# Optimization experiments

Measured on AMD Instinct MI355X. Metric: run time of the kernel, lower is better.

## Reference

```python
import jax, jax.numpy as jnp
import numpy as np

COLOR_CODE_NUMBER = 9

def _conv(x, w, b):
    # NCHW conv, 3x3, stride 1, padding 1 (SAME)
    y = jax.lax.conv_general_dilated(x, w, (1, 1), 'SAME',
                                     dimension_numbers=('NCHW', 'OIHW', 'NCHW'))
    return y + b[None, :, None, None]

def setup_inputs() -> dict:
    key = jax.random.key(0)
    ks = jax.random.split(key, 10)
    C, H, W = 256, 256, 256
    ms = 32
    s = 0.02
    x = jax.random.normal(ks[0], (1, C, H, W), dtype=jnp.float32)
    masks = jax.random.randint(ks[1], (COLOR_CODE_NUMBER, H, W), 0, 2, dtype=jnp.int32)
    w1 = jax.random.normal(ks[2], (128, 256, 3, 3), dtype=jnp.float32) * s
    b1 = jnp.zeros((128,), jnp.float32)
    w2 = jax.random.normal(ks[3], (64, 128, 3, 3), dtype=jnp.float32) * s
    b2 = jnp.zeros((64,), jnp.float32)
    w3 = jax.random.normal(ks[4], (ms, 64, 3, 3), dtype=jnp.float32) * s
    b3 = jnp.zeros((ms,), jnp.float32)
    fc_w = jax.random.normal(ks[5], (ms * ms, ms * ms), dtype=jnp.float32) * s
    fc_b = jnp.zeros((ms * ms,), jnp.float32)
    return {'x': x, 'masks': masks, 'w1': w1, 'b1': b1, 'w2': w2, 'b2': b2,
            'w3': w3, 'b3': b3, 'fc_w': fc_w, 'fc_b': fc_b}

def reference(x, masks, w1, b1, w2, b2, w3, b3, fc_w, fc_b):
    xb, xc, xh, xw = x.shape
    N = xh * xw
    K = masks.shape[0]
    xv = x.reshape(xc, N)                       # [C, N]
    m = masks.reshape(K, N)                     # [K, N] int
    fg = (m > 0).astype(x.dtype)                # [K, N]
    counts = fg.sum(axis=1)                     # [K]
    valid = counts >= 10.0                      # sum(mask) >= 10 for binary masks
    # per-mask gather -> mean-subtract -> scatter (sequential: later masks overwrite)
    fsm = xv
    for i in range(min(COLOR_CODE_NUMBER, K)):
        mean = (xv * fg[i]).sum(axis=1) / jnp.maximum(counts[i], 1.0)   # [C]
        sub = jnp.where(fg[i][None, :] > 0, xv - mean[:, None], fsm)
        fsm = jnp.where(valid[i], sub, fsm)
    # conv stack on mean-subtracted feature
    feat = fsm.reshape(xb, xc, xh, xw)
    feat = jax.nn.relu(_conv(feat, w1, b1))
    feat = jax.nn.relu(_conv(feat, w2, b2))
    feat = _conv(feat, w3, b3)                  # [1, ms, H, W]
    c = feat.shape[1]
    fv = feat.reshape(c, N)                     # [ms, N]
    # per-mask covariance + fc (vectorized over the 9 masks)
    fg1 = (m == 1).astype(feat.dtype)           # [K, N]
    cnt1 = fg1.sum(axis=1)                      # [K]
    masked = fv[None, :, :] * fg1[:, None, :]   # [K, ms, N]
    cov = jnp.einsum('kcn,kdn->kcd', masked, masked) / jnp.maximum(cnt1, 1.0)[:, None, None]
    trans = cov.reshape(K, c * c) @ fc_w.T + fc_b[None, :]              # [K, ms*ms]
    trans = jnp.where((cnt1 >= 10.0)[:, None], trans, jnp.zeros_like(trans))
    return trans, fsm
```

## Files before the change

kernel.cpp:

```cpp
#include <hip/hip_runtime.h>
#include <stdint.h>

#define N_PIX 65536
#define KM 9

typedef __bf16  bf16x8 __attribute__((ext_vector_type(8)));
typedef float   f32x4  __attribute__((ext_vector_type(4)));
typedef unsigned short ushort;

__device__ __forceinline__ ushort f2bf(float f) {
    uint32_t u = __builtin_bit_cast(uint32_t, f);
    uint32_t r = (u + 0x7FFFu + ((u >> 16) & 1u)) >> 16;
    return (ushort)r;
}

#define WS_BITS  0u
#define WS_CNT   262144u
#define WS_CNT1  262208u
#define WS_SUMS  262272u
#define WS_MEANS 271488u
#define WS_W1T   282624u
#define WS_W2T   872448u
#define WS_W3T   1019904u
#define WS_COV   1056768u
#define WS_XPAD  2097152u
#define WS_FV    2097152u
#define WS_PART  12582912u
#define WS_C1PAD 36173824u
#define WS_C2PAD 53212160u

template<int C>
__global__ void k_ring(ushort* p) {
    constexpr int CU = C / 2;
    int i = blockIdx.x * 256 + threadIdx.x;
    if (i >= 1028 * CU) return;
    int c = i % CU, px = i / CU;
    int row, col;
    if      (px < 258) { row = 0;   col = px; }
    else if (px < 516) { row = 257; col = px - 258; }
    else if (px < 772) { row = px - 516 + 1; col = 0; }
    else               { row = px - 772 + 1; col = 257; }
    ((uint32_t*)p)[(row * 258 + col) * CU + c] = 0u;
}

__global__ void k_pack(const int* __restrict__ masks, uint32_t* __restrict__ bits,
                       int* __restrict__ counts, int* __restrict__ cnt1) {
    int n = blockIdx.x * 256 + threadIdx.x;
    uint32_t fg = 0, f1 = 0;
#pragma unroll
    for (int k = 0; k < KM; ++k) {
        int m = masks[k * N_PIX + n];
        fg |= (uint32_t)(m > 0) << k;
        f1 |= (uint32_t)(m == 1) << k;
    }
    bits[n] = fg | (f1 << 16);
#pragma unroll
    for (int k = 0; k < KM; ++k) {
        unsigned long long b0 = __ballot((fg >> k) & 1);
        unsigned long long b1 = __ballot((f1 >> k) & 1);
        if ((threadIdx.x & 63) == 0) {
            atomicAdd(&counts[k], __popcll(b0));
            atomicAdd(&cnt1[k], __popcll(b1));
        }
    }
}

__global__ void k_sums(const float* __restrict__ x, const uint32_t* __restrict__ bits,
                       float* __restrict__ sums) {
    int c = blockIdx.x >> 4;
    int base = (blockIdx.x & 15) * 4096;
    float acc[KM];
#pragma unroll
    for (int k = 0; k < KM; ++k) acc[k] = 0.0f;
    const float* xc = x + (size_t)c * N_PIX;
    for (int i = 0; i < 16; ++i) {
        int px = base + i * 256 + threadIdx.x;
        float xv = xc[px];
        uint32_t b = bits[px];
#pragma unroll
        for (int k = 0; k < KM; ++k) acc[k] += ((b >> k) & 1) ? xv : 0.0f;
    }
#pragma unroll
    for (int k = 0; k < KM; ++k) {
        float v = acc[k];
        for (int off = 32; off; off >>= 1) v += __shfl_down(v, off);
        if ((threadIdx.x & 63) == 0) atomicAdd(&sums[k * 256 + c], v);
    }
}

__global__ void k_means(const float* __restrict__ sums, const int* __restrict__ counts,
                        float* __restrict__ means) {
    int k = blockIdx.x, c = threadIdx.x;
    means[k * 256 + c] = sums[k * 256 + c] / fmaxf((float)counts[k], 1.0f);
}

__global__ void k_fsm(const float* __restrict__ x, const uint32_t* __restrict__ bits,
                      const int* __restrict__ counts, const float* __restrict__ means,
                      float* __restrict__ fsm, ushort* __restrict__ xpad) {
    __shared__ float mst[256 * 12];
    int tid = threadIdx.x;
    for (int t = tid; t < KM * 256; t += 256) {
        int k = t >> 8, c = t & 255;
        mst[c * 12 + k] = means[t];
    }
    __syncthreads();
    uint32_t vm = 0;
#pragma unroll
    for (int k = 0; k < KM; ++k) vm |= (uint32_t)(counts[k] >= 10) << k;
    int px = blockIdx.x * 256 + tid;
    int c0 = blockIdx.y * 128;
    uint32_t sel = bits[px] & vm & 0x1FFu;
    int kl = 0; float have = 0.0f;
    if (sel) { kl = 31 - __clz((int)sel); have = 1.0f; }
    int y = px >> 8, xx = px & 255;
    size_t pbase = ((size_t)(y + 1) * 258 + (xx + 1)) * 256;
    for (int cb = 0; cb < 128; cb += 8) {
        int c = c0 + cb;
        uint32_t pk[4];
#pragma unroll
        for (int j = 0; j < 8; j += 2) {
            float v0 = x[(size_t)(c + j) * N_PIX + px]     - have * mst[(c + j) * 12 + kl];
            float v1 = x[(size_t)(c + j + 1) * N_PIX + px] - have * mst[(c + j + 1) * 12 + kl];
            fsm[(size_t)(c + j) * N_PIX + px] = v0;
            fsm[(size_t)(c + j + 1) * N_PIX + px] = v1;
            pk[j >> 1] = (uint32_t)f2bf(v0) | ((uint32_t)f2bf(v1) << 16);
        }
        uint4 w; w.x = pk[0]; w.y = pk[1]; w.z = pk[2]; w.w = pk[3];
        *(uint4*)&xpad[pbase + c] = w;
    }
}

__global__ void k_wpack(const float* __restrict__ w, ushort* __restrict__ wt,
                        int total, int OC, int IC) {
    int idx = blockIdx.x * 256 + threadIdx.x;
    if (idx >= total) return;
    int oc = idx / IC, ic = idx - oc * IC;
    const float* src = w + (size_t)idx * 9;
#pragma unroll
    for (int t = 0; t < 9; ++t)
        wt[((size_t)t * OC + oc) * IC + ic] = f2bf(src[t]);
}

template<int IC, int OC, int NT, int PXG, bool RELU, bool F32OUT>
__global__ __launch_bounds__(256) void k_convm(const ushort* __restrict__ xin,
                                               const ushort* __restrict__ wt,
                                               const float* __restrict__ bias,
                                               ushort* __restrict__ ypad,
                                               float* __restrict__ yf) {
    constexpr int NC   = IC / 32;
    constexpr int BPX  = 32 * PXG;
    constexpr int SEG  = 256 / BPX;
    constexpr int PXP  = BPX + 2;
    constexpr int RW   = PXP * 4;
    constexpr int UNITS = 3 * RW;
    constexpr int NCH  = (UNITS + 63) / 64;
    constexpr int NV   = (NCH + 3) / 4;
    static_assert(OC == 16 * NT * (4 / PXG), "tile mismatch");

    __shared__ ushort xs[NCH * 512];

    const int tid = threadIdx.x, lane = tid & 63, wv = tid >> 6;
    const int lo = lane & 15, kg = lane >> 4;
    const int y0 = blockIdx.x / SEG;
    const int x0 = (blockIdx.x % SEG) * BPX;
    const int wvpx = (wv % PXG) * 32;
    const int oc0  = (wv / PXG) * 16 * NT;

    uint32_t voff[NV];
#pragma unroll
    for (int j = 0; j < NV; ++j) {
        int ch = wv + j * 4;
        int u = ch * 64 + lane;
        u = (u < UNITS) ? u : (UNITS - 1);
        int row = u / RW;
        int rem = u - row * RW;
        int px = rem >> 2, icg = rem & 3;
        voff[j] = (uint32_t)(((y0 + row) * 258 + (x0 + px)) * IC + icg * 8);
    }

    const ushort* wlane = wt + (size_t)(oc0 + lo) * IC + kg * 8;
    const int abase = (wvpx + lo) * 32 + kg * 8;

    f32x4 acc[2][NT];
#pragma unroll
    for (int m = 0; m < 2; ++m)
#pragma unroll
        for (int n = 0; n < NT; ++n) acc[m][n] = (f32x4){0.f, 0.f, 0.f, 0.f};
    float bs[NT];
#pragma unroll
    for (int n = 0; n < NT; ++n) bs[n] = bias[oc0 + n * 16 + lo];

    uint4 sreg[NV];
#pragma unroll
    for (int j = 0; j < NV; ++j)
        if (wv + j * 4 < NCH) sreg[j] = *(const uint4*)(xin + voff[j]);

    for (int icc = 0; icc < NC; ++icc) {
#pragma unroll
        for (int j = 0; j < NV; ++j) {
            int ch = wv + j * 4;
            if (ch < NCH) *(uint4*)(xs + ch * 512 + lane * 8) = sreg[j];
        }
        __syncthreads();
        bf16x8 wf[9][NT];
#pragma unroll
        for (int tap = 0; tap < 9; ++tap)
#pragma unroll
            for (int n = 0; n < NT; ++n)
                wf[tap][n] = __builtin_bit_cast(bf16x8,
                    *(const uint4*)(wlane + ((size_t)tap * OC + n * 16) * IC + icc * 32));
        if (icc + 1 < NC) {
#pragma unroll
            for (int j = 0; j < NV; ++j)
                if (wv + j * 4 < NCH)
                    sreg[j] = *(const uint4*)(xin + voff[j] + (icc + 1) * 32);
        }
#pragma unroll
        for (int tr = 0; tr < 3; ++tr)
#pragma unroll
            for (int tc = 0; tc < 3; ++tc) {
                bf16x8 a0 = __builtin_bit_cast(bf16x8,
                    *(const uint4*)(xs + abase + (tr * PXP + tc) * 32));
                bf16x8 a1 = __builtin_bit_cast(bf16x8,
                    *(const uint4*)(xs + abase + (tr * PXP + tc) * 32 + 512));
#pragma unroll
                for (int n = 0; n < NT; ++n) {
                    acc[0][n] = __builtin_amdgcn_mfma_f32_16x16x32_bf16(a0, wf[tr * 3 + tc][n], acc[0][n], 0, 0, 0);
                    acc[1][n] = __builtin_amdgcn_mfma_f32_16x16x32_bf16(a1, wf[tr * 3 + tc][n], acc[1][n], 0, 0, 0);
                }
            }
        __syncthreads();
    }
#pragma unroll
    for (int m = 0; m < 2; ++m) {
        int pxl = x0 + wvpx + m * 16 + kg * 4;
#pragma unroll
        for (int n = 0; n < NT; ++n) {
            int oc = oc0 + n * 16 + lo;
#pragma unroll
            for (int r = 0; r < 4; ++r) {
                float v = acc[m][n][r] + bs[n];
                if (RELU) v = fmaxf(v, 0.0f);
                if (F32OUT) yf[((size_t)y0 * 256 + pxl + r) * OC + oc] = v;
                else        ypad[((size_t)(y0 + 1) * 258 + (pxl + r) + 1) * OC + oc] = f2bf(v);
            }
        }
    }
}

__global__ __launch_bounds__(256) void k_cov(const float* __restrict__ fv,
                                             const uint32_t* __restrict__ bits,
                                             float* __restrict__ part) {
    __shared__ float sf[32 * 257];
    __shared__ uint32_t sb[256];
    int px0 = blockIdx.x * 256;
    int tid = threadIdx.x;
    const float4* src = (const float4*)(fv + (size_t)(px0 + tid) * 32);
#pragma unroll
    for (int q = 0; q < 8; ++q) {
        float4 v = src[q];
        sf[(q * 4 + 0) * 257 + tid] = v.x;
        sf[(q * 4 + 1) * 257 + tid] = v.y;
        sf[(q * 4 + 2) * 257 + tid] = v.z;
        sf[(q * 4 + 3) * 257 + tid] = v.w;
    }
    sb[tid] = bits[px0 + tid] >> 16;
    __syncthreads();
    int c = tid >> 3;
    int d4 = (tid & 7) * 4;
    float a[KM][4];
#pragma unroll
    for (int k = 0; k < KM; ++k)
#pragma unroll
        for (int j = 0; j < 4; ++j) a[k][j] = 0.0f;
#pragma unroll 2
    for (int px = 0; px < 256; ++px) {
        float fc = sf[c * 257 + px];
        float f0 = sf[(d4 + 0) * 257 + px];
        float f1 = sf[(d4 + 1) * 257 + px];
        float f2 = sf[(d4 + 2) * 257 + px];
        float f3 = sf[(d4 + 3) * 257 + px];
        uint32_t b = sb[px];
#pragma unroll
        for (int k = 0; k < KM; ++k) {
            float fm = ((b >> k) & 1) ? fc : 0.0f;
            a[k][0] = fmaf(fm, f0, a[k][0]);
            a[k][1] = fmaf(fm, f1, a[k][1]);
            a[k][2] = fmaf(fm, f2, a[k][2]);
            a[k][3] = fmaf(fm, f3, a[k][3]);
        }
    }
    float* po = part + (size_t)blockIdx.x * 9216 + (c * 32 + d4);
#pragma unroll
    for (int k = 0; k < KM; ++k)
#pragma unroll
        for (int j = 0; j < 4; ++j) po[k * 1024 + j] = a[k][j];
}

__global__ void k_covred(const float* __restrict__ part, float* __restrict__ cov) {
    int p = blockIdx.x * 256 + threadIdx.x;
    float s = 0.0f;
    for (int b = 0; b < 256; ++b) s += part[(size_t)b * 9216 + p];
    cov[p] = s;
}

__global__ void k_fc(const float* __restrict__ cov, const int* __restrict__ cnt1,
                     const float* __restrict__ fcw, const float* __restrict__ fcb,
                     float* __restrict__ trans) {
    int k = blockIdx.x;
    int j = blockIdx.y * 256 + threadIdx.x;
    __shared__ float sc[1024];
    int c1 = cnt1[k];
    float inv = 1.0f / fmaxf((float)c1, 1.0f);
    for (int t = threadIdx.x; t < 1024; t += 256) sc[t] = cov[k * 1024 + t] * inv;
    __syncthreads();
    const float4* wrow = (const float4*)(fcw + (size_t)j * 1024);
    float acc = fcb[j];
#pragma unroll 4
    for (int i4 = 0; i4 < 256; ++i4) {
        float4 wv = wrow[i4];
        acc += sc[i4 * 4 + 0] * wv.x + sc[i4 * 4 + 1] * wv.y +
               sc[i4 * 4 + 2] * wv.z + sc[i4 * 4 + 3] * wv.w;
    }
    trans[k * 1024 + j] = (c1 >= 10) ? acc : 0.0f;
}

extern "C" void kernel_launch(void* const* d_in, const int* in_sizes, int n_in,
                              void* d_out, int out_size, void* d_ws, size_t ws_size,
                              hipStream_t stream) {
    const float* x     = (const float*)d_in[0];
    const int*   masks = (const int*)  d_in[1];
    const float* w1    = (const float*)d_in[2];
    const float* b1    = (const float*)d_in[3];
    const float* w2    = (const float*)d_in[4];
    const float* b2    = (const float*)d_in[5];
    const float* w3    = (const float*)d_in[6];
    const float* b3    = (const float*)d_in[7];
    const float* fcw   = (const float*)d_in[8];
    const float* fcb   = (const float*)d_in[9];

    float* out   = (float*)d_out;
    float* trans = out;
    float* fsm   = out + KM * 1024;

    char* ws = (char*)d_ws;
    uint32_t* bits = (uint32_t*)(ws + WS_BITS);
    int*   counts  = (int*)  (ws + WS_CNT);
    int*   cnt1    = (int*)  (ws + WS_CNT1);
    float* sums    = (float*)(ws + WS_SUMS);
    float* means   = (float*)(ws + WS_MEANS);
    ushort* w1t = (ushort*)(ws + WS_W1T);
    ushort* w2t = (ushort*)(ws + WS_W2T);
    ushort* w3t = (ushort*)(ws + WS_W3T);
    float* cov     = (float*)(ws + WS_COV);
    ushort* xpad  = (ushort*)(ws + WS_XPAD);
    ushort* c1pad = (ushort*)(ws + WS_C1PAD);
    ushort* c2pad = (ushort*)(ws + WS_C2PAD);
    float* fv      = (float*)(ws + WS_FV);
    float* part    = (float*)(ws + WS_PART);

    hipMemsetAsync(ws + WS_CNT, 0, 64 + 64 + 9216, stream);

    k_ring<256><<<(1028 * 128 + 255) / 256, 256, 0, stream>>>(xpad);
    k_ring<128><<<(1028 *  64 + 255) / 256, 256, 0, stream>>>(c1pad);
    k_ring< 64><<<(1028 *  32 + 255) / 256, 256, 0, stream>>>(c2pad);

    k_wpack<<<128, 256, 0, stream>>>(w1, w1t, 128 * 256, 128, 256);
    k_wpack<<< 32, 256, 0, stream>>>(w2, w2t,  64 * 128,  64, 128);
    k_wpack<<<  8, 256, 0, stream>>>(w3, w3t,  32 *  64,  32,  64);

    k_pack <<<256, 256, 0, stream>>>(masks, bits, counts, cnt1);
    k_sums <<<4096, 256, 0, stream>>>(x, bits, sums);
    k_means<<<KM, 256, 0, stream>>>(sums, counts, means);
    k_fsm  <<<dim3(256, 2), 256, 0, stream>>>(x, bits, counts, means, fsm, xpad);

    k_convm<256, 128, 4, 2, true,  false><<<1024, 256, 0, stream>>>(xpad,  w1t, b1, c1pad, nullptr);
    k_convm<128,  64, 4, 4, true,  false><<< 512, 256, 0, stream>>>(c1pad, w2t, b2, c2pad, nullptr);
    k_convm< 64,  32, 2, 4, false, true ><<< 512, 256, 0, stream>>>(c2pad, w3t, b3, nullptr, fv);

    k_cov   <<<256, 256, 0, stream>>>(fv, bits, part);
    k_covred<<<36, 256, 0, stream>>>(part, cov);
    k_fc    <<<dim3(KM, 4), 256, 0, stream>>>(cov, cnt1, fcw, fcb, trans);
}
```

Baseline: 705.6 us.

## Stream conv weight fragments with double buffer and retile conv2/conv3 to 64px blocks

The conv kernel stops preloading all nine taps of weight fragments into registers. It keeps a two-slot rolling buffer, loading the fragment for tap+2 while tap computes, and adds a launch bound of 4 blocks per CU to raise occupancy. Every layer now uses a fixed 64-pixel by 2-oc-group tiling, so conv2 and conv3 launch 1024 blocks with smaller NT. Fewer registers per thread in exchange for weight loads that sit closer to their use, which may expose latency, and more input halo reloads for the smaller layers.

New measurement: 680.9 us. -3.5%, faster.

```diff
diff --git a/kernel.cpp b/kernel.cpp
--- a/kernel.cpp
+++ b/kernel.cpp
@@ -141,30 +141,28 @@
         wt[((size_t)t * OC + oc) * IC + ic] = f2bf(src[t]);
 }
 
-template<int IC, int OC, int NT, int PXG, bool RELU, bool F32OUT>
-__global__ __launch_bounds__(256) void k_convm(const ushort* __restrict__ xin,
-                                               const ushort* __restrict__ wt,
-                                               const float* __restrict__ bias,
-                                               ushort* __restrict__ ypad,
-                                               float* __restrict__ yf) {
-    constexpr int NC   = IC / 32;
-    constexpr int BPX  = 32 * PXG;
-    constexpr int SEG  = 256 / BPX;
-    constexpr int PXP  = BPX + 2;
-    constexpr int RW   = PXP * 4;
+template<int IC, int OC, int NT, bool RELU, bool F32OUT>
+__global__ __launch_bounds__(256, 4) void k_convm(const ushort* __restrict__ xin,
+                                                  const ushort* __restrict__ wt,
+                                                  const float* __restrict__ bias,
+                                                  ushort* __restrict__ ypad,
+                                                  float* __restrict__ yf) {
+    constexpr int NC  = IC / 32;
+    constexpr int PXP = 66;
+    constexpr int RW  = PXP * 4;
     constexpr int UNITS = 3 * RW;
-    constexpr int NCH  = (UNITS + 63) / 64;
-    constexpr int NV   = (NCH + 3) / 4;
-    static_assert(OC == 16 * NT * (4 / PXG), "tile mismatch");
+    constexpr int NCH = (UNITS + 63) / 64;
+    constexpr int NV  = (NCH + 3) / 4;
+    static_assert(OC == NT * 32, "2 oc-groups of 16*NT");
 
     __shared__ ushort xs[NCH * 512];
 
     const int tid = threadIdx.x, lane = tid & 63, wv = tid >> 6;
     const int lo = lane & 15, kg = lane >> 4;
-    const int y0 = blockIdx.x / SEG;
-    const int x0 = (blockIdx.x % SEG) * BPX;
-    const int wvpx = (wv % PXG) * 32;
-    const int oc0  = (wv / PXG) * 16 * NT;
+    const int y0 = blockIdx.x >> 2;
+    const int x0 = (blockIdx.x & 3) << 6;
+    const int wvpx = (wv & 1) << 5;
+    const int oc0  = (wv >> 1) * NT * 16;
 
     uint32_t voff[NV];
 #pragma unroll
@@ -202,33 +200,40 @@
             if (ch < NCH) *(uint4*)(xs + ch * 512 + lane * 8) = sreg[j];
         }
         __syncthreads();
-        bf16x8 wf[9][NT];
-#pragma unroll
-        for (int tap = 0; tap < 9; ++tap)
-#pragma unroll
-            for (int n = 0; n < NT; ++n)
-                wf[tap][n] = __builtin_bit_cast(bf16x8,
-                    *(const uint4*)(wlane + ((size_t)tap * OC + n * 16) * IC + icc * 32));
         if (icc + 1 < NC) {
 #pragma unroll
             for (int j = 0; j < NV; ++j)
                 if (wv + j * 4 < NCH)
                     sreg[j] = *(const uint4*)(xin + voff[j] + (icc + 1) * 32);
         }
-#pragma unroll
-        for (int tr = 0; tr < 3; ++tr)
-#pragma unroll
-            for (int tc = 0; tc < 3; ++tc) {
-                bf16x8 a0 = __builtin_bit_cast(bf16x8,
-                    *(const uint4*)(xs + abase + (tr * PXP + tc) * 32));
-                bf16x8 a1 = __builtin_bit_cast(bf16x8,
-                    *(const uint4*)(xs + abase + (tr * PXP + tc) * 32 + 512));
+        const ushort* wicc = wlane + icc * 32;
+        uint4 wb0[NT], wb1[NT];
+#pragma unroll
+        for (int n = 0; n < NT; ++n) {
+            wb0[n] = *(const uint4*)(wicc + ((size_t)0 * OC + n * 16) * IC);
+            wb1[n] = *(const uint4*)(wicc + ((size_t)1 * OC + n * 16) * IC);
+        }
+#pragma unroll
+        for (int tap = 0; tap < 9; ++tap) {
+            const int tr = tap / 3, tc = tap % 3;
+            bf16x8 a0 = __builtin_bit_cast(bf16x8,
+                *(const uint4*)(xs + abase + (tr * PXP + tc) * 32));
+            bf16x8 a1 = __builtin_bit_cast(bf16x8,
+                *(const uint4*)(xs + abase + (tr * PXP + tc) * 32 + 512));
+#pragma unroll
+            for (int n = 0; n < NT; ++n) {
+                bf16x8 wfr = __builtin_bit_cast(bf16x8, (tap & 1) ? wb1[n] : wb0[n]);
+                acc[0][n] = __builtin_amdgcn_mfma_f32_16x16x32_bf16(a0, wfr, acc[0][n], 0, 0, 0);
+                acc[1][n] = __builtin_amdgcn_mfma_f32_16x16x32_bf16(a1, wfr, acc[1][n], 0, 0, 0);
+            }
+            if (tap + 2 < 9) {
 #pragma unroll
                 for (int n = 0; n < NT; ++n) {
-                    acc[0][n] = __builtin_amdgcn_mfma_f32_16x16x32_bf16(a0, wf[tr * 3 + tc][n], acc[0][n], 0, 0, 0);
-                    acc[1][n] = __builtin_amdgcn_mfma_f32_16x16x32_bf16(a1, wf[tr * 3 + tc][n], acc[1][n], 0, 0, 0);
+                    uint4 v = *(const uint4*)(wicc + ((size_t)(tap + 2) * OC + n * 16) * IC);
+                    if (tap & 1) wb1[n] = v; else wb0[n] = v;
                 }
             }
+        }
         __syncthreads();
     }
 #pragma unroll
@@ -374,9 +379,9 @@
     k_means<<<KM, 256, 0, stream>>>(sums, counts, means);
     k_fsm  <<<dim3(256, 2), 256, 0, stream>>>(x, bits, counts, means, fsm, xpad);
 
-    k_convm<256, 128, 4, 2, true,  false><<<1024, 256, 0, stream>>>(xpad,  w1t, b1, c1pad, nullptr);
-    k_convm<128,  64, 4, 4, true,  false><<< 512, 256, 0, stream>>>(c1pad, w2t, b2, c2pad, nullptr);
-    k_convm< 64,  32, 2, 4, false, true ><<< 512, 256, 0, stream>>>(c2pad, w3t, b3, nullptr, fv);
+    k_convm<256, 128, 4, true,  false><<<1024, 256, 0, stream>>>(xpad,  w1t, b1, c1pad, nullptr);
+    k_convm<128,  64, 2, true,  false><<<1024, 256, 0, stream>>>(c1pad, w2t, b2, c2pad, nullptr);
+    k_convm< 64,  32, 1, false, true ><<<1024, 256, 0, stream>>>(c2pad, w3t, b3, nullptr, fv);
 
     k_cov   <<<256, 256, 0, stream>>>(fv, bits, part);
     k_covred<<<36, 256, 0, stream>>>(part, cov);
```

## Retile conv kernel: stage weights in LDS, 128-pixel row tiles, split output channels

Applied to the files above, without the earlier changes.

The implicit-GEMM conv kernel is retiled. Each block now covers a 128-pixel row segment and a 64- or 32-channel output slice, with every wave handling 32 pixels across all channels of the slice. Weights for each input-channel chunk are staged into shared memory alongside the input tile, rather than each lane loading 9*NT weight fragments from global memory into registers. The aim is to cut redundant global weight traffic and register pressure, and launch_bounds(256,2) is added for occupancy. In exchange the kernel does more LDS reads per MFMA and uses more shared memory per block.

Measured after the change: 759.2 us. 1.08x slower.

```diff
diff --git a/kernel.cpp b/kernel.cpp
--- a/kernel.cpp
+++ b/kernel.cpp
@@ -141,45 +141,49 @@
         wt[((size_t)t * OC + oc) * IC + ic] = f2bf(src[t]);
 }
 
-template<int IC, int OC, int NT, int PXG, bool RELU, bool F32OUT>
-__global__ __launch_bounds__(256) void k_convm(const ushort* __restrict__ xin,
-                                               const ushort* __restrict__ wt,
-                                               const float* __restrict__ bias,
-                                               ushort* __restrict__ ypad,
-                                               float* __restrict__ yf) {
+template<int IC, int OCall, int OCB, bool RELU, bool F32OUT>
+__global__ __launch_bounds__(256, 2) void k_convm(const ushort* __restrict__ xin,
+                                                  const ushort* __restrict__ wt,
+                                                  const float* __restrict__ bias,
+                                                  ushort* __restrict__ ypad,
+                                                  float* __restrict__ yf) {
+    constexpr int NT   = OCB / 16;
     constexpr int NC   = IC / 32;
-    constexpr int BPX  = 32 * PXG;
-    constexpr int SEG  = 256 / BPX;
-    constexpr int PXP  = BPX + 2;
-    constexpr int RW   = PXP * 4;
-    constexpr int UNITS = 3 * RW;
-    constexpr int NCH  = (UNITS + 63) / 64;
-    constexpr int NV   = (NCH + 3) / 4;
-    static_assert(OC == 16 * NT * (4 / PXG), "tile mismatch");
-
-    __shared__ ushort xs[NCH * 512];
+    constexpr int TOTX = 3 * 130 * 4;
+    constexpr int NXV  = (TOTX + 255) / 256;
+    constexpr int TOTW = OCB * 36;
+    constexpr int NWV  = (TOTW + 255) / 256;
+
+    __shared__ ushort smem[TOTX * 8 + TOTW * 8];
+    ushort* xs = smem;
+    ushort* wl = smem + TOTX * 8;
 
     const int tid = threadIdx.x, lane = tid & 63, wv = tid >> 6;
     const int lo = lane & 15, kg = lane >> 4;
-    const int y0 = blockIdx.x / SEG;
-    const int x0 = (blockIdx.x % SEG) * BPX;
-    const int wvpx = (wv % PXG) * 32;
-    const int oc0  = (wv / PXG) * 16 * NT;
-
-    uint32_t voff[NV];
-#pragma unroll
-    for (int j = 0; j < NV; ++j) {
-        int ch = wv + j * 4;
-        int u = ch * 64 + lane;
-        u = (u < UNITS) ? u : (UNITS - 1);
-        int row = u / RW;
-        int rem = u - row * RW;
+    const int seg = blockIdx.x & 1;
+    const int y0  = (blockIdx.x >> 1) & 255;
+    const int ocg = blockIdx.x >> 9;
+    const int x0  = seg * 128;
+    const int oc0 = ocg * OCB;
+    const int wvpx = wv * 32;
+
+    uint32_t xoffg[NXV];
+#pragma unroll
+    for (int j = 0; j < NXV; ++j) {
+        int u = tid + j * 256;
+        int uu = (u < TOTX) ? u : 0;
+        int row = uu / 520, rem = uu - row * 520;
         int px = rem >> 2, icg = rem & 3;
-        voff[j] = (uint32_t)(((y0 + row) * 258 + (x0 + px)) * IC + icg * 8);
-    }
-
-    const ushort* wlane = wt + (size_t)(oc0 + lo) * IC + kg * 8;
-    const int abase = (wvpx + lo) * 32 + kg * 8;
+        xoffg[j] = (uint32_t)(((y0 + row) * 258 + (x0 + px)) * IC + icg * 8);
+    }
+    uint32_t woffg[NWV];
+#pragma unroll
+    for (int j = 0; j < NWV; ++j) {
+        int u = tid + j * 256;
+        int uu = (u < TOTW) ? u : 0;
+        int tap = uu / (OCB * 4), r = uu - tap * (OCB * 4);
+        woffg[j] = (uint32_t)((tap * OCall + oc0 + (r >> 2)) * IC + (r & 3) * 8);
+    }
 
     f32x4 acc[2][NT];
 #pragma unroll
@@ -190,45 +194,52 @@
 #pragma unroll
     for (int n = 0; n < NT; ++n) bs[n] = bias[oc0 + n * 16 + lo];
 
-    uint4 sreg[NV];
-#pragma unroll
-    for (int j = 0; j < NV; ++j)
-        if (wv + j * 4 < NCH) sreg[j] = *(const uint4*)(xin + voff[j]);
+    const int xbase = (wvpx + lo) * 32 + kg * 8;
+    const int wbase = lo * 32 + kg * 8;
+
+    uint4 xr[NXV], wr[NWV];
+#pragma unroll
+    for (int j = 0; j < NXV; ++j)
+        if (tid + j * 256 < TOTX) xr[j] = *(const uint4*)(xin + xoffg[j]);
+#pragma unroll
+    for (int j = 0; j < NWV; ++j)
+        if (tid + j * 256 < TOTW) wr[j] = *(const uint4*)(wt + woffg[j]);
 
     for (int icc = 0; icc < NC; ++icc) {
 #pragma unroll
-        for (int j = 0; j < NV; ++j) {
-            int ch = wv + j * 4;
-            if (ch < NCH) *(uint4*)(xs + ch * 512 + lane * 8) = sreg[j];
+        for (int j = 0; j < NXV; ++j) {
+            int u = tid + j * 256;
+            if (u < TOTX) *(uint4*)(xs + u * 8) = xr[j];
+        }
+#pragma unroll
+        for (int j = 0; j < NWV; ++j) {
+            int u = tid + j * 256;
+            if (u < TOTW) *(uint4*)(wl + u * 8) = wr[j];
         }
         __syncthreads();
-        bf16x8 wf[9][NT];
-#pragma unroll
-        for (int tap = 0; tap < 9; ++tap)
-#pragma unroll
-            for (int n = 0; n < NT; ++n)
-                wf[tap][n] = __builtin_bit_cast(bf16x8,
-                    *(const uint4*)(wlane + ((size_t)tap * OC + n * 16) * IC + icc * 32));
         if (icc + 1 < NC) {
 #pragma unroll
-            for (int j = 0; j < NV; ++j)
-                if (wv + j * 4 < NCH)
-                    sreg[j] = *(const uint4*)(xin + voff[j] + (icc + 1) * 32);
-        }
-#pragma unroll
-        for (int tr = 0; tr < 3; ++tr)
-#pragma unroll
-            for (int tc = 0; tc < 3; ++tc) {
-                bf16x8 a0 = __builtin_bit_cast(bf16x8,
-                    *(const uint4*)(xs + abase + (tr * PXP + tc) * 32));
-                bf16x8 a1 = __builtin_bit_cast(bf16x8,
-                    *(const uint4*)(xs + abase + (tr * PXP + tc) * 32 + 512));
-#pragma unroll
-                for (int n = 0; n < NT; ++n) {
-                    acc[0][n] = __builtin_amdgcn_mfma_f32_16x16x32_bf16(a0, wf[tr * 3 + tc][n], acc[0][n], 0, 0, 0);
-                    acc[1][n] = __builtin_amdgcn_mfma_f32_16x16x32_bf16(a1, wf[tr * 3 + tc][n], acc[1][n], 0, 0, 0);
-                }
+            for (int j = 0; j < NXV; ++j)
+                if (tid + j * 256 < TOTX) xr[j] = *(const uint4*)(xin + xoffg[j] + (icc + 1) * 32);
+#pragma unroll
+            for (int j = 0; j < NWV; ++j)
+                if (tid + j * 256 < TOTW) wr[j] = *(const uint4*)(wt + woffg[j] + (icc + 1) * 32);
+        }
+#pragma unroll
+        for (int tap = 0; tap < 9; ++tap) {
+            const int tr = tap / 3, tc = tap % 3;
+            bf16x8 a0 = __builtin_bit_cast(bf16x8,
+                *(const uint4*)(xs + xbase + (tr * 130 + tc) * 32));
+            bf16x8 a1 = __builtin_bit_cast(bf16x8,
+                *(const uint4*)(xs + xbase + (tr * 130 + tc) * 32 + 512));
+#pragma unroll
+            for (int n = 0; n < NT; ++n) {
+                bf16x8 b = __builtin_bit_cast(bf16x8,
+                    *(const uint4*)(wl + wbase + tap * (OCB * 32) + n * 512));
+                acc[0][n] = __builtin_amdgcn_mfma_f32_16x16x32_bf16(a0, b, acc[0][n], 0, 0, 0);
+                acc[1][n] = __builtin_amdgcn_mfma_f32_16x16x32_bf16(a1, b, acc[1][n], 0, 0, 0);
             }
+        }
         __syncthreads();
     }
 #pragma unroll
@@ -241,8 +252,8 @@
             for (int r = 0; r < 4; ++r) {
                 float v = acc[m][n][r] + bs[n];
                 if (RELU) v = fmaxf(v, 0.0f);
-                if (F32OUT) yf[((size_t)y0 * 256 + pxl + r) * OC + oc] = v;
-                else        ypad[((size_t)(y0 + 1) * 258 + (pxl + r) + 1) * OC + oc] = f2bf(v);
+                if (F32OUT) yf[((size_t)y0 * 256 + pxl + r) * OCall + oc] = v;
+                else        ypad[((size_t)(y0 + 1) * 258 + (pxl + r) + 1) * OCall + oc] = f2bf(v);
             }
         }
     }
@@ -374,9 +385,9 @@
     k_means<<<KM, 256, 0, stream>>>(sums, counts, means);
     k_fsm  <<<dim3(256, 2), 256, 0, stream>>>(x, bits, counts, means, fsm, xpad);
 
-    k_convm<256, 128, 4, 2, true,  false><<<1024, 256, 0, stream>>>(xpad,  w1t, b1, c1pad, nullptr);
-    k_convm<128,  64, 4, 4, true,  false><<< 512, 256, 0, stream>>>(c1pad, w2t, b2, c2pad, nullptr);
-    k_convm< 64,  32, 2, 4, false, true ><<< 512, 256, 0, stream>>>(c2pad, w3t, b3, nullptr, fv);
+    k_convm<256, 128, 64, true,  false><<<1024, 256, 0, stream>>>(xpad,  w1t, b1, c1pad, nullptr);
+    k_convm<128,  64, 64, true,  false><<< 512, 256, 0, stream>>>(c1pad, w2t, b2, c2pad, nullptr);
+    k_convm< 64,  32, 32, false, true ><<< 512, 256, 0, stream>>>(c2pad, w3t, b3, nullptr, fv);
 
     k_cov   <<<256, 256, 0, stream>>>(fv, bits, part);
     k_covred<<<36, 256, 0, stream>>>(part, cov);
```
